# Performance work log

Measured on AMD Instinct MI355X. Metric: run time of the kernel, lower is better.

The kernel has to match this reference:

```python
import jax, jax.numpy as jnp
import numpy as np

GROUPS = 32
EPS = 1e-5

def setup_inputs() -> dict:
    key = jax.random.key(0)
    k1, k2, k3 = jax.random.split(key, 3)
    C = 512
    x = jax.random.normal(k1, (4, C, 64, 64), dtype=jnp.float32)
    gn_weight = jnp.ones((C,), jnp.float32)
    gn_bias = jnp.zeros((C,), jnp.float32)
    qkv_weight = jax.random.normal(k2, (3 * C, C), jnp.float32) * (1.0 / np.sqrt(C))
    proj_weight = jax.random.normal(k3, (C, C), jnp.float32) * (1.0 / np.sqrt(C))
    proj_bias = jnp.zeros((C,), jnp.float32)
    return {"x": x, "gn_weight": gn_weight, "gn_bias": gn_bias,
            "qkv_weight": qkv_weight, "proj_weight": proj_weight, "proj_bias": proj_bias}

def reference(x, gn_weight, gn_bias, qkv_weight, proj_weight, proj_bias):
    n, c, h, w = x.shape
    residue = x
    # GroupNorm(32, c): normalize over (c//32 channels * h * w) per group
    xg = x.reshape(n, GROUPS, -1)
    mu = xg.mean(axis=-1, keepdims=True)
    var = xg.var(axis=-1, keepdims=True)
    xn = (xg - mu) * jax.lax.rsqrt(var + EPS)
    xn = xn.reshape(n, c, h, w) * gn_weight[None, :, None, None] + gn_bias[None, :, None, None]
    # tokens: [n, T, c] with T = h*w
    t = xn.reshape(n, c, h * w).transpose(0, 2, 1)
    # qkv linear (no bias), n_heads = 1 so head_size = c
    qkv = jnp.einsum('ntc,dc->ntd', t, qkv_weight)
    q, k, v = jnp.split(qkv, 3, axis=-1)
    scale = 1.0 / np.sqrt(c)
    scores = jnp.einsum('nqc,nkc->nqk', q, k) * scale  # [n, T, T]
    weights = jax.nn.softmax(scores, axis=-1)
    out = jnp.einsum('nqk,nkc->nqc', weights, v)
    out = jnp.einsum('ntc,dc->ntd', out, proj_weight) + proj_bias
    out = out.transpose(0, 2, 1).reshape(n, c, h, w)
    return out + residue
```

## Files before the change

kernel.cpp:

```cpp
#include <hip/hip_runtime.h>
#include <hip/hip_bf16.h>

typedef __bf16 bf16;
typedef __bf16 bf16x8 __attribute__((ext_vector_type(8)));
typedef float f32x4 __attribute__((ext_vector_type(4)));

__device__ __forceinline__ void gload_lds16(const bf16* g, bf16* l) {
    __builtin_amdgcn_global_load_lds(
        (const __attribute__((address_space(1))) void*)g,
        (__attribute__((address_space(3))) void*)l, 16, 0, 0);
}

__global__ __launch_bounds__(256) void k_gnstats(const float* __restrict__ x,
                                                 float2* __restrict__ stats) {
    const int g = blockIdx.x;
    const float4* p = (const float4*)(x + (long)g * 65536);
    float s = 0.f, ss = 0.f;
    #pragma unroll 8
    for (int i = 0; i < 64; ++i) {
        float4 v = p[threadIdx.x + i * 256];
        s  += v.x + v.y + v.z + v.w;
        ss += v.x * v.x + v.y * v.y + v.z * v.z + v.w * v.w;
    }
    #pragma unroll
    for (int off = 32; off >= 1; off >>= 1) {
        s  += __shfl_down(s, off);
        ss += __shfl_down(ss, off);
    }
    __shared__ float rs[4], rss[4];
    if ((threadIdx.x & 63) == 0) { rs[threadIdx.x >> 6] = s; rss[threadIdx.x >> 6] = ss; }
    __syncthreads();
    if (threadIdx.x == 0) {
        float S  = rs[0] + rs[1] + rs[2] + rs[3];
        float SS = rss[0] + rss[1] + rss[2] + rss[3];
        float mu = S * (1.f / 65536.f);
        float var = SS * (1.f / 65536.f) - mu * mu;
        stats[g] = make_float2(mu, rsqrtf(var + 1e-5f));
    }
}

__global__ __launch_bounds__(256) void k_norm_t(const float* __restrict__ x,
                                                const float* __restrict__ w,
                                                const float* __restrict__ b,
                                                const float2* __restrict__ stats,
                                                bf16* __restrict__ t) {
    __shared__ float tile[64][65];
    const int bid = blockIdx.x;
    const int n = bid >> 9, rem = bid & 511;
    const int s0 = (rem >> 3) * 64, c0 = (rem & 7) * 64;
    const int tid = threadIdx.x;
    const int sl = tid & 63, cq = tid >> 6;
    #pragma unroll
    for (int i = 0; i < 16; ++i) {
        const int cl = cq * 16 + i;
        const int c = c0 + cl;
        const float2 st = stats[n * 32 + (c >> 4)];
        const float v = x[((long)(n * 512 + c)) * 4096 + s0 + sl];
        tile[cl][sl] = (v - st.x) * st.y * w[c] + b[c];
    }
    __syncthreads();
    #pragma unroll
    for (int i = 0; i < 16; ++i) {
        const int sl2 = cq * 16 + i;
        const int cl2 = tid & 63;
        t[((long)(n * 4096 + s0 + sl2)) * 512 + c0 + cl2] = (bf16)tile[cl2][sl2];
    }
}

__global__ __launch_bounds__(256) void k_convw(const float* __restrict__ qw,
                                               const float* __restrict__ pw,
                                               bf16* __restrict__ qwb,
                                               bf16* __restrict__ pwb) {
    const int i = blockIdx.x * 256 + threadIdx.x;
    if (i < 786432) {
        float v = qw[i];
        if (i < 512 * 512) v *= 0.06376281516217733f;
        qwb[i] = (bf16)v;
    } else {
        const int j = i - 786432;
        pwb[j] = (bf16)pw[j];
    }
}

__global__ __launch_bounds__(256) void k_vt(const bf16* __restrict__ qkv,
                                            bf16* __restrict__ Vt) {
    __shared__ bf16 tile[64][66];
    const int bid = blockIdx.x;
    const int n = bid >> 9, rem = bid & 511;
    const int s0 = (rem >> 3) * 64, d0 = (rem & 7) * 64;
    const int tid = threadIdx.x;
    #pragma unroll
    for (int i = 0; i < 16; ++i) {
        const int sl = (tid >> 6) * 16 + i;
        const int dl = tid & 63;
        tile[sl][dl] = qkv[((long)(n * 4096 + s0 + sl)) * 1536 + 1024 + d0 + dl];
    }
    __syncthreads();
    #pragma unroll
    for (int i = 0; i < 16; ++i) {
        const int dl = (tid >> 6) * 16 + i;
        const int sl = tid & 63;
        Vt[((long)(n * 512 + d0 + dl)) * 4096 + s0 + sl] = tile[sl][dl];
    }
}

__global__ __launch_bounds__(512, 1) void k_flashpv(
    const bf16* __restrict__ S, const bf16* __restrict__ Vt,
    bf16* __restrict__ O) {
    __shared__ bf16 Bs[2][512 * 64];
    __shared__ bf16 As[64 * 64];
    __shared__ float sstat[64];
    const int t = threadIdx.x;
    const int w = t >> 6, l = t & 63, lr = l & 15, lg = l >> 4;
    const int r = t >> 3, c8 = t & 7, r7 = r & 7;
    const int lr7 = lr & 7;
    const long z = blockIdx.y;
    const int bx = blockIdx.x;

    const bf16* Sg = S + z * ((long)4096 * 4096) + (long)(bx * 64 + r) * 4096 + c8 * 8;
    const bf16* Vg = Vt + z * ((long)512 * 4096) + (long)r * 4096 + (c8 ^ r7) * 8;

    auto issueB = [&](int tile, int buf) {
        bf16* lp = Bs[buf];
        #pragma unroll
        for (int u = 0; u < 8; ++u)
            gload_lds16(Vg + (long)u * 64 * 4096 + tile * 64, lp + u * 4096 + t * 8);
    };

    f32x4 acc[4][4];
    #pragma unroll
    for (int i = 0; i < 4; ++i)
        #pragma unroll
        for (int n = 0; n < 4; ++n) acc[i][n] = f32x4{0.f, 0.f, 0.f, 0.f};

    float m_run = -1e30f, l_run = 0.f;
    bf16x8 pa;
    float scale = 0.f;

    auto stats = [&](bf16x8 sv) {
        float fv[8];
        #pragma unroll
        for (int j = 0; j < 8; ++j) fv[j] = (float)sv[j];
        float tmax = fv[0];
        #pragma unroll
        for (int j = 1; j < 8; ++j) tmax = fmaxf(tmax, fv[j]);
        tmax = fmaxf(tmax, __shfl_xor(tmax, 1));
        tmax = fmaxf(tmax, __shfl_xor(tmax, 2));
        tmax = fmaxf(tmax, __shfl_xor(tmax, 4));
        float mnew, scl;
        if (tmax > m_run + 8.f) { mnew = tmax; scl = exp2f(m_run - tmax); }
        else                    { mnew = m_run; scl = 1.f; }
        float ts = 0.f;
        #pragma unroll
        for (int j = 0; j < 8; ++j) { fv[j] = exp2f(fv[j] - mnew); ts += fv[j]; }
        ts += __shfl_xor(ts, 1);
        ts += __shfl_xor(ts, 2);
        ts += __shfl_xor(ts, 4);
        l_run = l_run * scl + ts;
        m_run = mnew;
        #pragma unroll
        for (int j = 0; j < 8; ++j) pa[j] = (bf16)fv[j];
        scale = scl;
    };

    bf16x8 sv0 = *(const bf16x8*)(Sg);
    issueB(0, 0);
    stats(sv0);

    for (int ti = 0; ti < 64; ++ti) {
        __builtin_amdgcn_s_barrier();
        asm volatile("" ::: "memory");
        *(bf16x8*)(As + r * 64 + ((c8 ^ r7) * 8)) = pa;
        if (c8 == 0) sstat[r] = scale;
        bf16x8 sv;
        if (ti < 63) {
            sv = *(const bf16x8*)(Sg + (ti + 1) * 64);
            issueB(ti + 1, (ti + 1) & 1);
            asm volatile("s_waitcnt vmcnt(9) lgkmcnt(0)" ::: "memory");
        } else {
            asm volatile("s_waitcnt vmcnt(0) lgkmcnt(0)" ::: "memory");
        }
        __builtin_amdgcn_sched_barrier(0);
        __builtin_amdgcn_s_barrier();
        asm volatile("" ::: "memory");

        #pragma unroll
        for (int mi = 0; mi < 4; ++mi) {
            float4 sc = *(const float4*)&sstat[mi * 16 + lg * 4];
            if (sc.x != 1.f || sc.y != 1.f || sc.z != 1.f || sc.w != 1.f) {
                f32x4 scv = {sc.x, sc.y, sc.z, sc.w};
                #pragma unroll
                for (int n = 0; n < 4; ++n) acc[mi][n] *= scv;
            }
        }

        const bf16* Bsb = Bs[ti & 1];
        __builtin_amdgcn_s_setprio(1);
        #pragma unroll
        for (int kk = 0; kk < 2; ++kk) {
            bf16x8 af[4], bf[4];
            #pragma unroll
            for (int mi = 0; mi < 4; ++mi)
                af[mi] = *(const bf16x8*)(As + (mi * 16 + lr) * 64 + (((kk * 4 + lg) ^ lr7) * 8));
            #pragma unroll
            for (int n = 0; n < 4; ++n)
                bf[n] = *(const bf16x8*)(Bsb + (w * 64 + n * 16 + lr) * 64 + (((kk * 4 + lg) ^ lr7) * 8));
            #pragma unroll
            for (int mi = 0; mi < 4; ++mi)
                #pragma unroll
                for (int n = 0; n < 4; ++n)
                    acc[mi][n] = __builtin_amdgcn_mfma_f32_16x16x32_bf16(af[mi], bf[n], acc[mi][n], 0, 0, 0);
        }
        __builtin_amdgcn_s_setprio(0);

        if (ti < 63) stats(sv);
    }

    __builtin_amdgcn_s_barrier();
    asm volatile("" ::: "memory");
    if (c8 == 0) sstat[r] = l_run;
    asm volatile("s_waitcnt lgkmcnt(0)" ::: "memory");
    __builtin_amdgcn_s_barrier();
    asm volatile("" ::: "memory");

    bf16* Oz = O + z * ((long)4096 * 512);
    #pragma unroll
    for (int mi = 0; mi < 4; ++mi) {
        float4 lv = *(const float4*)&sstat[mi * 16 + lg * 4];
        float inv0 = 1.f / lv.x, inv1 = 1.f / lv.y, inv2 = 1.f / lv.z, inv3 = 1.f / lv.w;
        #pragma unroll
        for (int n = 0; n < 4; ++n) {
            const long base = (long)(bx * 64 + mi * 16 + lg * 4) * 512 + w * 64 + n * 16 + lr;
            Oz[base]           = (bf16)(acc[mi][n][0] * inv0);
            Oz[base + 512]     = (bf16)(acc[mi][n][1] * inv1);
            Oz[base + 1024]    = (bf16)(acc[mi][n][2] * inv2);
            Oz[base + 1536]    = (bf16)(acc[mi][n][3] * inv3);
        }
    }
}

#define PH(mh, kk, S_, WN)                                                         \
  {                                                                                \
    if ((mh) == 0) {                                                               \
      _Pragma("unroll")                                                            \
      for (int n = 0; n < 4; ++n) {                                                \
        int row = wn * 64 + n * 16 + lr;                                           \
        int cg = lg ^ (row & 3);                                                   \
        bfr[n] = *(const bf16x8*)(BsT + (kk) * 8192 + row * 32 + cg * 8);          \
      }                                                                            \
    }                                                                              \
    _Pragma("unroll")                                                              \
    for (int i = 0; i < 4; ++i) {                                                  \
      int row = wm * 128 + ((mh) * 4 + i) * 16 + lr;                               \
      int cg = lg ^ (row & 3);                                                     \
      af[i] = *(const bf16x8*)(AsT + (kk) * 8192 + row * 32 + cg * 8);             \
    }                                                                              \
    if ((S_) >= 0) issue_unit(S_);                                                 \
    __builtin_amdgcn_s_barrier();                                                  \
    asm volatile("" ::: "memory");                                                 \
    __builtin_amdgcn_s_setprio(1);                                                 \
    _Pragma("unroll")                                                              \
    for (int i = 0; i < 4; ++i)                                                    \
      _Pragma("unroll")                                                            \
      for (int n = 0; n < 4; ++n)                                                  \
        acc[(mh) * 4 + i][n] =                                                     \
            __builtin_amdgcn_mfma_f32_16x16x32_bf16(af[i], bfr[n],                 \
                                                    acc[(mh) * 4 + i][n], 0, 0, 0);\
    __builtin_amdgcn_s_setprio(0);                                                 \
    if constexpr ((WN) >= 0)                                                       \
      asm volatile("s_waitcnt vmcnt(%0)" ::"i"(WN) : "memory");                    \
    __builtin_amdgcn_s_barrier();                                                  \
    asm volatile("" ::: "memory");                                                 \
  }

__global__ __launch_bounds__(512, 2) void gemm256(
    const bf16* __restrict__ A, int lda, long aZ,
    const bf16* __restrict__ B, int ldb, long bZ,
    bf16* __restrict__ C, int ldc, long cZ, int K) {
    __shared__ bf16 As[2 * 2 * 256 * 32];
    __shared__ bf16 Bs[2 * 2 * 256 * 32];
    const int t = threadIdx.x;
    const int wid = t >> 6, l = t & 63;
    const int wm = wid >> 2, wn = wid & 3;
    const int lr = l & 15;
    const int lg = l >> 4;
    const long z = blockIdx.z;

    const int gx = gridDim.x;
    int nwg = gx * gridDim.y;
    int flat = blockIdx.y * gx + blockIdx.x;
    if ((nwg & 7) == 0) { int qq = nwg >> 3; flat = (flat & 7) * qq + (flat >> 3); }
    const int bx = flat % gx, by = flat / gx;

    const bf16* Ab = A + z * aZ + (long)bx * 256 * lda;
    const bf16* Bb = B + z * bZ + (long)by * 256 * ldb;

    const int NT = K >> 6;
    const int NT4 = NT << 2;

    f32x4 acc[8][4];
    #pragma unroll
    for (int i = 0; i < 8; ++i)
        #pragma unroll
        for (int n = 0; n < 4; ++n) acc[i][n] = f32x4{0.f, 0.f, 0.f, 0.f};

    const int srow = t >> 2;
    const int scg0 = t & 3;

    auto issue_unit = [&](int s) {
        int ti = s >> 2, idx = s & 3;
        int kh = idx >> 1, isB = idx & 1;
        const bf16* g = isB ? Bb : Ab;
        int ld = isB ? ldb : lda;
        bf16* lp = (isB ? Bs : As) + ((ti & 1) * 2 + kh) * 8192;
        int k0 = ti * 64 + kh * 32;
        #pragma unroll
        for (int j = 0; j < 2; ++j) {
            int row = j * 128 + srow;
            int cg = scg0 ^ (row & 3);
            gload_lds16(g + (long)row * ld + k0 + cg * 8, lp + (j * 512 + t) * 8);
        }
    };

    #pragma unroll
    for (int s = 0; s < 6; ++s) issue_unit(s);
    asm volatile("s_waitcnt vmcnt(8)" ::: "memory");
    __builtin_amdgcn_s_barrier();
    asm volatile("" ::: "memory");

    bf16x8 bfr[4], af[4];

    for (int ti = 0; ti < NT - 2; ++ti) {
        const bf16* AsT = As + (ti & 1) * 16384;
        const bf16* BsT = Bs + (ti & 1) * 16384;
        const int sb = 4 * ti + 6;
        PH(0, 0, sb + 0, -1)
        PH(1, 0, sb + 1, 8)
        PH(0, 1, sb + 2, -1)
        PH(1, 1, sb + 3, 8)
    }
    {
        const bf16* AsT = As + ((NT - 2) & 1) * 16384;
        const bf16* BsT = Bs + ((NT - 2) & 1) * 16384;
        PH(0, 0, NT4 - 2, -1)
        PH(1, 0, NT4 - 1, 8)
        PH(0, 1, -1, -1)
        PH(1, 1, -1, 4)
    }
    {
        const bf16* AsT = As + ((NT - 1) & 1) * 16384;
        const bf16* BsT = Bs + ((NT - 1) & 1) * 16384;
        PH(0, 0, -1, -1)
        PH(1, 0, -1, 0)
        PH(0, 1, -1, -1)
        PH(1, 1, -1, -1)
    }

    const int row0 = bx * 256 + wm * 128;
    const int col0 = by * 256 + wn * 64;
    const int rq = lg * 4;
    bf16* Cz = C + z * cZ;
    #pragma unroll
    for (int i = 0; i < 8; ++i)
        #pragma unroll
        for (int n = 0; n < 4; ++n) {
            const int col = col0 + n * 16 + lr;
            #pragma unroll
            for (int r = 0; r < 4; ++r)
                Cz[(long)(row0 + i * 16 + rq + r) * ldc + col] = (bf16)acc[i][n][r];
        }
}

#define PH128(nh, kk, S_, WN)                                                      \
  {                                                                                \
    if ((nh) == 0) {                                                               \
      _Pragma("unroll")                                                            \
      for (int i = 0; i < 4; ++i) {                                                \
        int row = wm * 64 + i * 16 + lr;                                           \
        int cg = lg ^ (row & 3);                                                   \
        af[i] = *(const bf16x8*)(AsT + (kk) * 8192 + row * 32 + cg * 8);           \
      }                                                                            \
    }                                                                              \
    _Pragma("unroll")                                                              \
    for (int j = 0; j < 2; ++j) {                                                  \
      int row = wn * 64 + ((nh) * 2 + j) * 16 + lr;                                \
      int cg = lg ^ (row & 3);                                                     \
      bfr[j] = *(const bf16x8*)(BsT + (kk) * 4096 + row * 32 + cg * 8);            \
    }                                                                              \
    if ((S_) >= 0) issue_unit(S_);                                                 \
    __builtin_amdgcn_s_barrier();                                                  \
    asm volatile("" ::: "memory");                                                 \
    __builtin_amdgcn_s_setprio(1);                                                 \
    _Pragma("unroll")                                                              \
    for (int i = 0; i < 4; ++i)                                                    \
      _Pragma("unroll")                                                            \
      for (int j = 0; j < 2; ++j)                                                  \
        acc[i][(nh) * 2 + j] =                                                     \
            __builtin_amdgcn_mfma_f32_16x16x32_bf16(af[i], bfr[j],                 \
                                                    acc[i][(nh) * 2 + j], 0, 0, 0);\
    __builtin_amdgcn_s_setprio(0);                                                 \
    if constexpr ((WN) >= 0)                                                       \
      asm volatile("s_waitcnt vmcnt(%0)" ::"i"(WN) : "memory");                    \
    __builtin_amdgcn_s_barrier();                                                  \
    asm volatile("" ::: "memory");                                                 \
  }

template <int EPI>
__global__ __launch_bounds__(512, 2) void gemm_n128(
    const bf16* __restrict__ A, int lda, long aZ,
    const bf16* __restrict__ B, int ldb, long bZ,
    void* __restrict__ Cvp, int ldc, long cZ, int K,
    const float* __restrict__ bias) {
    __shared__ bf16 As[2 * 2 * 256 * 32];
    __shared__ bf16 Bs[2 * 2 * 128 * 32];
    const int t = threadIdx.x;
    const int wid = t >> 6, l = t & 63;
    const int wm = wid >> 1, wn = wid & 1;
    const int lr = l & 15;
    const int lg = l >> 4;
    const long z = blockIdx.z;

    const int gx = gridDim.x;
    int nwg = gx * gridDim.y;
    int flat = blockIdx.y * gx + blockIdx.x;
    if ((nwg & 7) == 0) { int qq = nwg >> 3; flat = (flat & 7) * qq + (flat >> 3); }
    const int bx = flat % gx, by = flat / gx;

    const bf16* Ab = A + z * aZ + (long)bx * 256 * lda;
    const bf16* Bb = B + z * bZ + (long)by * 128 * ldb;

    const int NT = K >> 6;
    const int NT4 = NT << 2;

    f32x4 acc[4][4];
    #pragma unroll
    for (int i = 0; i < 4; ++i)
        #pragma unroll
        for (int n = 0; n < 4; ++n) acc[i][n] = f32x4{0.f, 0.f, 0.f, 0.f};

    const int srow = t >> 2;
    const int scg0 = t & 3;

    auto issue_unit = [&](int s) {
        int ti = s >> 2, idx = s & 3;
        int kh = idx >> 1, isB = idx & 1;
        int k0 = ti * 64 + kh * 32;
        if (isB) {
            bf16* lp = Bs + ((ti & 1) * 2 + kh) * 4096;
            int cg = scg0 ^ (srow & 3);
            gload_lds16(Bb + (long)srow * ldb + k0 + cg * 8, lp + t * 8);
        } else {
            bf16* lp = As + ((ti & 1) * 2 + kh) * 8192;
            #pragma unroll
            for (int j = 0; j < 2; ++j) {
                int row = j * 128 + srow;
                int cg = scg0 ^ (row & 3);
                gload_lds16(Ab + (long)row * lda + k0 + cg * 8, lp + (j * 512 + t) * 8);
            }
        }
    };

    #pragma unroll
    for (int s = 0; s < 6; ++s) issue_unit(s);
    asm volatile("s_waitcnt vmcnt(6)" ::: "memory");
    __builtin_amdgcn_s_barrier();
    asm volatile("" ::: "memory");

    bf16x8 bfr[2], af[4];

    for (int ti = 0; ti < NT - 2; ++ti) {
        const bf16* AsT = As + (ti & 1) * 16384;
        const bf16* BsT = Bs + (ti & 1) * 8192;
        const int sb = 4 * ti + 6;
        PH128(0, 0, sb + 0, -1)
        PH128(1, 0, sb + 1, 6)
        PH128(0, 1, sb + 2, -1)
        PH128(1, 1, sb + 3, 6)
    }
    {
        const bf16* AsT = As + ((NT - 2) & 1) * 16384;
        const bf16* BsT = Bs + ((NT - 2) & 1) * 8192;
        PH128(0, 0, NT4 - 2, -1)
        PH128(1, 0, NT4 - 1, 6)
        PH128(0, 1, -1, -1)
        PH128(1, 1, -1, 3)
    }
    {
        const bf16* AsT = As + ((NT - 1) & 1) * 16384;
        const bf16* BsT = Bs + ((NT - 1) & 1) * 8192;
        PH128(0, 0, -1, -1)
        PH128(1, 0, -1, 0)
        PH128(0, 1, -1, -1)
        PH128(1, 1, -1, -1)
    }

    const int row0 = bx * 256 + wm * 64;
    const int col0 = by * 128 + wn * 64;
    const int rq = lg * 4;
    if (EPI == 2) {
        float* C = (float*)Cvp + z * cZ;
        #pragma unroll
        for (int i = 0; i < 4; ++i)
            #pragma unroll
            for (int n = 0; n < 4; ++n) {
                const int col = col0 + n * 16 + lr;
                #pragma unroll
                for (int r = 0; r < 4; ++r)
                    C[(long)(row0 + i * 16 + rq + r) * ldc + col] = acc[i][n][r] + bias[col];
            }
    } else {
        bf16* C = (bf16*)Cvp + z * cZ;
        #pragma unroll
        for (int i = 0; i < 4; ++i)
            #pragma unroll
            for (int n = 0; n < 4; ++n) {
                const int col = col0 + n * 16 + lr;
                #pragma unroll
                for (int r = 0; r < 4; ++r)
                    C[(long)(row0 + i * 16 + rq + r) * ldc + col] = (bf16)acc[i][n][r];
            }
    }
}

__global__ __launch_bounds__(256) void k_final(const float* __restrict__ pb,
                                               const float* __restrict__ x,
                                               float* __restrict__ out) {
    __shared__ float tile[64][65];
    const int bid = blockIdx.x;
    const int n = bid >> 9, rem = bid & 511;
    const int s0 = (rem >> 3) * 64, c0 = (rem & 7) * 64;
    const int tid = threadIdx.x;
    #pragma unroll
    for (int i = 0; i < 16; ++i) {
        const int sl = (tid >> 6) * 16 + i;
        const int cl = tid & 63;
        tile[sl][cl] = pb[((long)(n * 4096 + s0 + sl)) * 512 + c0 + cl];
    }
    __syncthreads();
    #pragma unroll
    for (int i = 0; i < 16; ++i) {
        const int cl = (tid >> 6) * 16 + i;
        const int sl = tid & 63;
        const long oi = ((long)(n * 512 + c0 + cl)) * 4096 + s0 + sl;
        out[oi] = tile[sl][cl] + x[oi];
    }
}

extern "C" void kernel_launch(void* const* d_in, const int* in_sizes, int n_in,
                              void* d_out, int out_size, void* d_ws, size_t ws_size,
                              hipStream_t stream) {
    const float* x     = (const float*)d_in[0];
    const float* gnw   = (const float*)d_in[1];
    const float* gnb   = (const float*)d_in[2];
    const float* qkvw  = (const float*)d_in[3];
    const float* projw = (const float*)d_in[4];
    const float* projb = (const float*)d_in[5];

    char* ws = (char*)d_ws;
    size_t off = 0;
    auto alloc = [&](size_t bytes) {
        void* p = ws + off;
        off += (bytes + 255) & ~(size_t)255;
        return p;
    };
    bf16*   qwb   = (bf16*)alloc((size_t)1536 * 512 * 2);
    bf16*   pwb   = (bf16*)alloc((size_t)512 * 512 * 2);
    float2* stats = (float2*)alloc((size_t)128 * 8);
    bf16*   tbuf  = (bf16*)alloc((size_t)16384 * 512 * 2);
    bf16*   qkv   = (bf16*)alloc((size_t)16384 * 1536 * 2);
    bf16*   Vt    = (bf16*)alloc((size_t)4 * 512 * 4096 * 2);
    const size_t SSZ = (size_t)4096 * 4096 * 2;
    const size_t fixed = off;
    int g = 1;
    if (ws_size >= fixed + 4 * SSZ) g = 4;
    else if (ws_size >= fixed + 2 * SSZ) g = 2;
    bf16* Sbuf = (bf16*)alloc(g * SSZ);

    k_gnstats<<<128, 256, 0, stream>>>(x, stats);
    k_norm_t<<<2048, 256, 0, stream>>>(x, gnw, gnb, stats, tbuf);
    k_convw<<<4096, 256, 0, stream>>>(qkvw, projw, qwb, pwb);

    gemm256<<<dim3(64, 6, 1), 512, 0, stream>>>(
        tbuf, 512, 0, qwb, 512, 0, qkv, 1536, 0, 512);

    k_vt<<<2048, 256, 0, stream>>>(qkv, Vt);

    const long TS = (long)4096 * 1536;
    for (int g0 = 0; g0 < 4; g0 += g) {
        gemm256<<<dim3(16, 16, g), 512, 0, stream>>>(
            qkv + (long)g0 * TS, 1536, TS,
            qkv + (long)g0 * TS + 512, 1536, TS,
            Sbuf, 4096, (long)4096 * 4096, 512);
        k_flashpv<<<dim3(64, g), 512, 0, stream>>>(
            Sbuf, Vt + (long)g0 * 512 * 4096, tbuf + (long)g0 * 4096 * 512);
    }

    gemm_n128<2><<<dim3(64, 4, 1), 512, 0, stream>>>(
        tbuf, 512, 0, pwb, 512, 0, (float*)Sbuf, 512, 0, 512, projb);

    k_final<<<2048, 256, 0, stream>>>((float*)Sbuf, x, (float*)d_out);
}
```

Baseline: 331.4 us.

## Split flash PV kernel across two head-dimension halves with 256-thread blocks

Measured after the change: 337.7 us. About the same (+1.9%).

```diff
diff --git a/kernel.cpp b/kernel.cpp
--- a/kernel.cpp
+++ b/kernel.cpp
@@ -104,27 +104,29 @@
     }
 }
 
-__global__ __launch_bounds__(512, 1) void k_flashpv(
+__global__ __launch_bounds__(256, 2) void k_flashpv(
     const bf16* __restrict__ S, const bf16* __restrict__ Vt,
     bf16* __restrict__ O) {
-    __shared__ bf16 Bs[2][512 * 64];
+    __shared__ bf16 Bs[2][256 * 64];
     __shared__ bf16 As[64 * 64];
     __shared__ float sstat[64];
     const int t = threadIdx.x;
     const int w = t >> 6, l = t & 63, lr = l & 15, lg = l >> 4;
-    const int r = t >> 3, c8 = t & 7, r7 = r & 7;
+    const int r = t >> 2, c4 = t & 3, r7 = r & 7;
+    const int vr = t >> 3, vc8 = t & 7, vr7 = vr & 7;
     const int lr7 = lr & 7;
-    const long z = blockIdx.y;
+    const long z = blockIdx.z;
     const int bx = blockIdx.x;
-
-    const bf16* Sg = S + z * ((long)4096 * 4096) + (long)(bx * 64 + r) * 4096 + c8 * 8;
-    const bf16* Vg = Vt + z * ((long)512 * 4096) + (long)r * 4096 + (c8 ^ r7) * 8;
+    const int dh = blockIdx.y;
+
+    const bf16* Sg = S + z * ((long)4096 * 4096) + (long)(bx * 64 + r) * 4096 + c4 * 16;
+    const bf16* Vg = Vt + z * ((long)512 * 4096) + (long)(dh * 256 + vr) * 4096 + (vc8 ^ vr7) * 8;
 
     auto issueB = [&](int tile, int buf) {
         bf16* lp = Bs[buf];
         #pragma unroll
         for (int u = 0; u < 8; ++u)
-            gload_lds16(Vg + (long)u * 64 * 4096 + tile * 64, lp + u * 4096 + t * 8);
+            gload_lds16(Vg + (long)u * 32 * 4096 + tile * 64, lp + u * 2048 + t * 8);
     };
 
     f32x4 acc[4][4];
@@ -134,49 +136,50 @@
         for (int n = 0; n < 4; ++n) acc[i][n] = f32x4{0.f, 0.f, 0.f, 0.f};
 
     float m_run = -1e30f, l_run = 0.f;
-    bf16x8 pa;
+    bf16x8 pa0, pa1;
     float scale = 0.f;
 
-    auto stats = [&](bf16x8 sv) {
-        float fv[8];
-        #pragma unroll
-        for (int j = 0; j < 8; ++j) fv[j] = (float)sv[j];
+    auto stats = [&](bf16x8 sa, bf16x8 sb) {
+        float fv[16];
+        #pragma unroll
+        for (int j = 0; j < 8; ++j) { fv[j] = (float)sa[j]; fv[8 + j] = (float)sb[j]; }
         float tmax = fv[0];
         #pragma unroll
-        for (int j = 1; j < 8; ++j) tmax = fmaxf(tmax, fv[j]);
+        for (int j = 1; j < 16; ++j) tmax = fmaxf(tmax, fv[j]);
         tmax = fmaxf(tmax, __shfl_xor(tmax, 1));
         tmax = fmaxf(tmax, __shfl_xor(tmax, 2));
-        tmax = fmaxf(tmax, __shfl_xor(tmax, 4));
         float mnew, scl;
         if (tmax > m_run + 8.f) { mnew = tmax; scl = exp2f(m_run - tmax); }
         else                    { mnew = m_run; scl = 1.f; }
         float ts = 0.f;
         #pragma unroll
-        for (int j = 0; j < 8; ++j) { fv[j] = exp2f(fv[j] - mnew); ts += fv[j]; }
+        for (int j = 0; j < 16; ++j) { fv[j] = exp2f(fv[j] - mnew); ts += fv[j]; }
         ts += __shfl_xor(ts, 1);
         ts += __shfl_xor(ts, 2);
-        ts += __shfl_xor(ts, 4);
         l_run = l_run * scl + ts;
         m_run = mnew;
         #pragma unroll
-        for (int j = 0; j < 8; ++j) pa[j] = (bf16)fv[j];
+        for (int j = 0; j < 8; ++j) { pa0[j] = (bf16)fv[j]; pa1[j] = (bf16)fv[8 + j]; }
         scale = scl;
     };
 
-    bf16x8 sv0 = *(const bf16x8*)(Sg);
+    bf16x8 sa0 = *(const bf16x8*)(Sg);
+    bf16x8 sb0 = *(const bf16x8*)(Sg + 8);
     issueB(0, 0);
-    stats(sv0);
+    stats(sa0, sb0);
 
     for (int ti = 0; ti < 64; ++ti) {
         __builtin_amdgcn_s_barrier();
         asm volatile("" ::: "memory");
-        *(bf16x8*)(As + r * 64 + ((c8 ^ r7) * 8)) = pa;
-        if (c8 == 0) sstat[r] = scale;
-        bf16x8 sv;
+        *(bf16x8*)(As + r * 64 + (((c4 * 2) ^ r7) * 8)) = pa0;
+        *(bf16x8*)(As + r * 64 + (((c4 * 2 + 1) ^ r7) * 8)) = pa1;
+        if (c4 == 0) sstat[r] = scale;
+        bf16x8 sa, sb;
         if (ti < 63) {
-            sv = *(const bf16x8*)(Sg + (ti + 1) * 64);
+            sa = *(const bf16x8*)(Sg + (ti + 1) * 64);
+            sb = *(const bf16x8*)(Sg + (ti + 1) * 64 + 8);
             issueB(ti + 1, (ti + 1) & 1);
-            asm volatile("s_waitcnt vmcnt(9) lgkmcnt(0)" ::: "memory");
+            asm volatile("s_waitcnt vmcnt(10) lgkmcnt(0)" ::: "memory");
         } else {
             asm volatile("s_waitcnt vmcnt(0) lgkmcnt(0)" ::: "memory");
         }
@@ -213,12 +216,12 @@
         }
         __builtin_amdgcn_s_setprio(0);
 
-        if (ti < 63) stats(sv);
+        if (ti < 63) stats(sa, sb);
     }
 
     __builtin_amdgcn_s_barrier();
     asm volatile("" ::: "memory");
-    if (c8 == 0) sstat[r] = l_run;
+    if (c4 == 0) sstat[r] = l_run;
     asm volatile("s_waitcnt lgkmcnt(0)" ::: "memory");
     __builtin_amdgcn_s_barrier();
     asm volatile("" ::: "memory");
@@ -230,7 +233,7 @@
         float inv0 = 1.f / lv.x, inv1 = 1.f / lv.y, inv2 = 1.f / lv.z, inv3 = 1.f / lv.w;
         #pragma unroll
         for (int n = 0; n < 4; ++n) {
-            const long base = (long)(bx * 64 + mi * 16 + lg * 4) * 512 + w * 64 + n * 16 + lr;
+            const long base = (long)(bx * 64 + mi * 16 + lg * 4) * 512 + dh * 256 + w * 64 + n * 16 + lr;
             Oz[base]           = (bf16)(acc[mi][n][0] * inv0);
             Oz[base + 512]     = (bf16)(acc[mi][n][1] * inv1);
             Oz[base + 1024]    = (bf16)(acc[mi][n][2] * inv2);
@@ -591,7 +594,7 @@
             qkv + (long)g0 * TS, 1536, TS,
             qkv + (long)g0 * TS + 512, 1536, TS,
             Sbuf, 4096, (long)4096 * 4096, 512);
-        k_flashpv<<<dim3(64, g), 512, 0, stream>>>(
+        k_flashpv<<<dim3(64, 2, g), 256, 0, stream>>>(
             Sbuf, Vt + (long)g0 * 512 * 4096, tbuf + (long)g0 * 4096 * 512);
     }
 
```

## Fuse exp and row-sum into QK^T GEMM epilogue, make PV a plain GEMM

Applied to the files above, without the earlier changes.

After: 312.5 us. 5.7% less time.

```diff
diff --git a/kernel.cpp b/kernel.cpp
--- a/kernel.cpp
+++ b/kernel.cpp
@@ -101,141 +101,6 @@
         const int dl = (tid >> 6) * 16 + i;
         const int sl = tid & 63;
         Vt[((long)(n * 512 + d0 + dl)) * 4096 + s0 + sl] = tile[sl][dl];
-    }
-}
-
-__global__ __launch_bounds__(512, 1) void k_flashpv(
-    const bf16* __restrict__ S, const bf16* __restrict__ Vt,
-    bf16* __restrict__ O) {
-    __shared__ bf16 Bs[2][512 * 64];
-    __shared__ bf16 As[64 * 64];
-    __shared__ float sstat[64];
-    const int t = threadIdx.x;
-    const int w = t >> 6, l = t & 63, lr = l & 15, lg = l >> 4;
-    const int r = t >> 3, c8 = t & 7, r7 = r & 7;
-    const int lr7 = lr & 7;
-    const long z = blockIdx.y;
-    const int bx = blockIdx.x;
-
-    const bf16* Sg = S + z * ((long)4096 * 4096) + (long)(bx * 64 + r) * 4096 + c8 * 8;
-    const bf16* Vg = Vt + z * ((long)512 * 4096) + (long)r * 4096 + (c8 ^ r7) * 8;
-
-    auto issueB = [&](int tile, int buf) {
-        bf16* lp = Bs[buf];
-        #pragma unroll
-        for (int u = 0; u < 8; ++u)
-            gload_lds16(Vg + (long)u * 64 * 4096 + tile * 64, lp + u * 4096 + t * 8);
-    };
-
-    f32x4 acc[4][4];
-    #pragma unroll
-    for (int i = 0; i < 4; ++i)
-        #pragma unroll
-        for (int n = 0; n < 4; ++n) acc[i][n] = f32x4{0.f, 0.f, 0.f, 0.f};
-
-    float m_run = -1e30f, l_run = 0.f;
-    bf16x8 pa;
-    float scale = 0.f;
-
-    auto stats = [&](bf16x8 sv) {
-        float fv[8];
-        #pragma unroll
-        for (int j = 0; j < 8; ++j) fv[j] = (float)sv[j];
-        float tmax = fv[0];
-        #pragma unroll
-        for (int j = 1; j < 8; ++j) tmax = fmaxf(tmax, fv[j]);
-        tmax = fmaxf(tmax, __shfl_xor(tmax, 1));
-        tmax = fmaxf(tmax, __shfl_xor(tmax, 2));
-        tmax = fmaxf(tmax, __shfl_xor(tmax, 4));
-        float mnew, scl;
-        if (tmax > m_run + 8.f) { mnew = tmax; scl = exp2f(m_run - tmax); }
-        else                    { mnew = m_run; scl = 1.f; }
-        float ts = 0.f;
-        #pragma unroll
-        for (int j = 0; j < 8; ++j) { fv[j] = exp2f(fv[j] - mnew); ts += fv[j]; }
-        ts += __shfl_xor(ts, 1);
-        ts += __shfl_xor(ts, 2);
-        ts += __shfl_xor(ts, 4);
-        l_run = l_run * scl + ts;
-        m_run = mnew;
-        #pragma unroll
-        for (int j = 0; j < 8; ++j) pa[j] = (bf16)fv[j];
-        scale = scl;
-    };
-
-    bf16x8 sv0 = *(const bf16x8*)(Sg);
-    issueB(0, 0);
-    stats(sv0);
-
-    for (int ti = 0; ti < 64; ++ti) {
-        __builtin_amdgcn_s_barrier();
-        asm volatile("" ::: "memory");
-        *(bf16x8*)(As + r * 64 + ((c8 ^ r7) * 8)) = pa;
-        if (c8 == 0) sstat[r] = scale;
-        bf16x8 sv;
-        if (ti < 63) {
-            sv = *(const bf16x8*)(Sg + (ti + 1) * 64);
-            issueB(ti + 1, (ti + 1) & 1);
-            asm volatile("s_waitcnt vmcnt(9) lgkmcnt(0)" ::: "memory");
-        } else {
-            asm volatile("s_waitcnt vmcnt(0) lgkmcnt(0)" ::: "memory");
-        }
-        __builtin_amdgcn_sched_barrier(0);
-        __builtin_amdgcn_s_barrier();
-        asm volatile("" ::: "memory");
-
-        #pragma unroll
-        for (int mi = 0; mi < 4; ++mi) {
-            float4 sc = *(const float4*)&sstat[mi * 16 + lg * 4];
-            if (sc.x != 1.f || sc.y != 1.f || sc.z != 1.f || sc.w != 1.f) {
-                f32x4 scv = {sc.x, sc.y, sc.z, sc.w};
-                #pragma unroll
-                for (int n = 0; n < 4; ++n) acc[mi][n] *= scv;
-            }
-        }
-
-        const bf16* Bsb = Bs[ti & 1];
-        __builtin_amdgcn_s_setprio(1);
-        #pragma unroll
-        for (int kk = 0; kk < 2; ++kk) {
-            bf16x8 af[4], bf[4];
-            #pragma unroll
-            for (int mi = 0; mi < 4; ++mi)
-                af[mi] = *(const bf16x8*)(As + (mi * 16 + lr) * 64 + (((kk * 4 + lg) ^ lr7) * 8));
-            #pragma unroll
-            for (int n = 0; n < 4; ++n)
-                bf[n] = *(const bf16x8*)(Bsb + (w * 64 + n * 16 + lr) * 64 + (((kk * 4 + lg) ^ lr7) * 8));
-            #pragma unroll
-            for (int mi = 0; mi < 4; ++mi)
-                #pragma unroll
-                for (int n = 0; n < 4; ++n)
-                    acc[mi][n] = __builtin_amdgcn_mfma_f32_16x16x32_bf16(af[mi], bf[n], acc[mi][n], 0, 0, 0);
-        }
-        __builtin_amdgcn_s_setprio(0);
-
-        if (ti < 63) stats(sv);
-    }
-
-    __builtin_amdgcn_s_barrier();
-    asm volatile("" ::: "memory");
-    if (c8 == 0) sstat[r] = l_run;
-    asm volatile("s_waitcnt lgkmcnt(0)" ::: "memory");
-    __builtin_amdgcn_s_barrier();
-    asm volatile("" ::: "memory");
-
-    bf16* Oz = O + z * ((long)4096 * 512);
-    #pragma unroll
-    for (int mi = 0; mi < 4; ++mi) {
-        float4 lv = *(const float4*)&sstat[mi * 16 + lg * 4];
-        float inv0 = 1.f / lv.x, inv1 = 1.f / lv.y, inv2 = 1.f / lv.z, inv3 = 1.f / lv.w;
-        #pragma unroll
-        for (int n = 0; n < 4; ++n) {
-            const long base = (long)(bx * 64 + mi * 16 + lg * 4) * 512 + w * 64 + n * 16 + lr;
-            Oz[base]           = (bf16)(acc[mi][n][0] * inv0);
-            Oz[base + 512]     = (bf16)(acc[mi][n][1] * inv1);
-            Oz[base + 1024]    = (bf16)(acc[mi][n][2] * inv2);
-            Oz[base + 1536]    = (bf16)(acc[mi][n][3] * inv3);
-        }
     }
 }
 
@@ -273,10 +138,12 @@
     asm volatile("" ::: "memory");                                                 \
   }
 
+template <int EPI>
 __global__ __launch_bounds__(512, 2) void gemm256(
     const bf16* __restrict__ A, int lda, long aZ,
     const bf16* __restrict__ B, int ldb, long bZ,
-    bf16* __restrict__ C, int ldc, long cZ, int K) {
+    bf16* __restrict__ C, int ldc, long cZ, int K,
+    float* __restrict__ Lp) {
     __shared__ bf16 As[2 * 2 * 256 * 32];
     __shared__ bf16 Bs[2 * 2 * 256 * 32];
     const int t = threadIdx.x;
@@ -360,15 +227,146 @@
     const int col0 = by * 256 + wn * 64;
     const int rq = lg * 4;
     bf16* Cz = C + z * cZ;
-    #pragma unroll
-    for (int i = 0; i < 8; ++i)
+
+    if (EPI == 1) {
+        float rs[8][4];
+        #pragma unroll
+        for (int i = 0; i < 8; ++i)
+            #pragma unroll
+            for (int r = 0; r < 4; ++r) rs[i][r] = 0.f;
+        #pragma unroll
+        for (int i = 0; i < 8; ++i)
+            #pragma unroll
+            for (int n = 0; n < 4; ++n) {
+                const int col = col0 + n * 16 + lr;
+                #pragma unroll
+                for (int r = 0; r < 4; ++r) {
+                    float p = exp2f(acc[i][n][r]);
+                    rs[i][r] += p;
+                    Cz[(long)(row0 + i * 16 + rq + r) * ldc + col] = (bf16)p;
+                }
+            }
+        #pragma unroll
+        for (int i = 0; i < 8; ++i)
+            #pragma unroll
+            for (int r = 0; r < 4; ++r) {
+                float s = rs[i][r];
+                s += __shfl_xor(s, 1);
+                s += __shfl_xor(s, 2);
+                s += __shfl_xor(s, 4);
+                s += __shfl_xor(s, 8);
+                rs[i][r] = s;
+            }
+        float* lsf = (float*)As;
+        if (lr == 0) {
+            #pragma unroll
+            for (int i = 0; i < 8; ++i)
+                #pragma unroll
+                for (int r = 0; r < 4; ++r)
+                    lsf[wn * 256 + wm * 128 + i * 16 + lg * 4 + r] = rs[i][r];
+        }
+        __syncthreads();
+        if (t < 256) {
+            float v = lsf[t] + lsf[256 + t] + lsf[512 + t] + lsf[768 + t];
+            Lp[((long)z * 16 + by) * 4096 + bx * 256 + t] = v;
+        }
+    } else {
+        #pragma unroll
+        for (int i = 0; i < 8; ++i)
+            #pragma unroll
+            for (int n = 0; n < 4; ++n) {
+                const int col = col0 + n * 16 + lr;
+                #pragma unroll
+                for (int r = 0; r < 4; ++r)
+                    Cz[(long)(row0 + i * 16 + rq + r) * ldc + col] = (bf16)acc[i][n][r];
+            }
+    }
+}
+
+__global__ __launch_bounds__(512, 1) void k_pv(
+    const bf16* __restrict__ P, const float* __restrict__ Lp,
+    const bf16* __restrict__ Vt, bf16* __restrict__ O) {
+    __shared__ bf16 Bs[2][512 * 64];
+    __shared__ bf16 As[2][64 * 64];
+    __shared__ float linv[64];
+    const int t = threadIdx.x;
+    const int w = t >> 6, l = t & 63, lr = l & 15, lg = l >> 4;
+    const int lr7 = lr & 7;
+    const int sr = t >> 3, sc8 = t & 7, sr7 = sr & 7;
+    const long z = blockIdx.y;
+    const int bx = blockIdx.x;
+
+    const bf16* Pg = P + z * ((long)4096 * 4096) + (long)(bx * 64 + sr) * 4096 + (sc8 ^ sr7) * 8;
+    const bf16* Vg = Vt + z * ((long)512 * 4096) + (long)sr * 4096 + (sc8 ^ sr7) * 8;
+
+    auto issue = [&](int tile, int buf) {
+        gload_lds16(Pg + tile * 64, As[buf] + t * 8);
+        #pragma unroll
+        for (int u = 0; u < 8; ++u)
+            gload_lds16(Vg + (long)u * 64 * 4096 + tile * 64, Bs[buf] + u * 4096 + t * 8);
+    };
+
+    if (t < 64) {
+        const float* lpp = Lp + z * 16 * 4096 + bx * 64 + t;
+        float s = 0.f;
+        #pragma unroll
+        for (int j = 0; j < 16; ++j) s += lpp[j * 4096];
+        linv[t] = 1.f / s;
+    }
+
+    f32x4 acc[4][4];
+    #pragma unroll
+    for (int i = 0; i < 4; ++i)
+        #pragma unroll
+        for (int n = 0; n < 4; ++n) acc[i][n] = f32x4{0.f, 0.f, 0.f, 0.f};
+
+    issue(0, 0);
+    issue(1, 1);
+
+    for (int ti = 0; ti < 64; ++ti) {
+        if (ti < 63) { asm volatile("s_waitcnt vmcnt(9)" ::: "memory"); }
+        else         { asm volatile("s_waitcnt vmcnt(0)" ::: "memory"); }
+        __builtin_amdgcn_s_barrier();
+        asm volatile("" ::: "memory");
+
+        const bf16* Asb = As[ti & 1];
+        const bf16* Bsb = Bs[ti & 1];
+        __builtin_amdgcn_s_setprio(1);
+        #pragma unroll
+        for (int kk = 0; kk < 2; ++kk) {
+            bf16x8 af[4], bfv[4];
+            #pragma unroll
+            for (int mi = 0; mi < 4; ++mi)
+                af[mi] = *(const bf16x8*)(Asb + (mi * 16 + lr) * 64 + (((kk * 4 + lg) ^ lr7) * 8));
+            #pragma unroll
+            for (int n = 0; n < 4; ++n)
+                bfv[n] = *(const bf16x8*)(Bsb + (w * 64 + n * 16 + lr) * 64 + (((kk * 4 + lg) ^ lr7) * 8));
+            #pragma unroll
+            for (int mi = 0; mi < 4; ++mi)
+                #pragma unroll
+                for (int n = 0; n < 4; ++n)
+                    acc[mi][n] = __builtin_amdgcn_mfma_f32_16x16x32_bf16(af[mi], bfv[n], acc[mi][n], 0, 0, 0);
+        }
+        __builtin_amdgcn_s_setprio(0);
+
+        __builtin_amdgcn_s_barrier();
+        asm volatile("" ::: "memory");
+        if (ti < 62) issue(ti + 2, ti & 1);
+    }
+
+    bf16* Oz = O + z * ((long)4096 * 512);
+    #pragma unroll
+    for (int mi = 0; mi < 4; ++mi) {
+        float4 lv = *(const float4*)&linv[mi * 16 + lg * 4];
         #pragma unroll
         for (int n = 0; n < 4; ++n) {
-            const int col = col0 + n * 16 + lr;
-            #pragma unroll
-            for (int r = 0; r < 4; ++r)
-                Cz[(long)(row0 + i * 16 + rq + r) * ldc + col] = (bf16)acc[i][n][r];
+            const long base = (long)(bx * 64 + mi * 16 + lg * 4) * 512 + w * 64 + n * 16 + lr;
+            Oz[base]        = (bf16)(acc[mi][n][0] * lv.x);
+            Oz[base + 512]  = (bf16)(acc[mi][n][1] * lv.y);
+            Oz[base + 1024] = (bf16)(acc[mi][n][2] * lv.z);
+            Oz[base + 1536] = (bf16)(acc[mi][n][3] * lv.w);
         }
+    }
 }
 
 #define PH128(nh, kk, S_, WN)                                                      \
@@ -569,6 +567,7 @@
     bf16*   tbuf  = (bf16*)alloc((size_t)16384 * 512 * 2);
     bf16*   qkv   = (bf16*)alloc((size_t)16384 * 1536 * 2);
     bf16*   Vt    = (bf16*)alloc((size_t)4 * 512 * 4096 * 2);
+    float*  Lpart = (float*)alloc((size_t)4 * 16 * 4096 * 4);
     const size_t SSZ = (size_t)4096 * 4096 * 2;
     const size_t fixed = off;
     int g = 1;
@@ -580,19 +579,19 @@
     k_norm_t<<<2048, 256, 0, stream>>>(x, gnw, gnb, stats, tbuf);
     k_convw<<<4096, 256, 0, stream>>>(qkvw, projw, qwb, pwb);
 
-    gemm256<<<dim3(64, 6, 1), 512, 0, stream>>>(
-        tbuf, 512, 0, qwb, 512, 0, qkv, 1536, 0, 512);
+    gemm256<0><<<dim3(64, 6, 1), 512, 0, stream>>>(
+        tbuf, 512, 0, qwb, 512, 0, qkv, 1536, 0, 512, nullptr);
 
     k_vt<<<2048, 256, 0, stream>>>(qkv, Vt);
 
     const long TS = (long)4096 * 1536;
     for (int g0 = 0; g0 < 4; g0 += g) {
-        gemm256<<<dim3(16, 16, g), 512, 0, stream>>>(
+        gemm256<1><<<dim3(16, 16, g), 512, 0, stream>>>(
             qkv + (long)g0 * TS, 1536, TS,
             qkv + (long)g0 * TS + 512, 1536, TS,
-            Sbuf, 4096, (long)4096 * 4096, 512);
-        k_flashpv<<<dim3(64, g), 512, 0, stream>>>(
-            Sbuf, Vt + (long)g0 * 512 * 4096, tbuf + (long)g0 * 4096 * 512);
+            Sbuf, 4096, (long)4096 * 4096, 512, Lpart);
+        k_pv<<<dim3(64, g), 512, 0, stream>>>(
+            Sbuf, Lpart, Vt + (long)g0 * 512 * 4096, tbuf + (long)g0 * 4096 * 512);
     }
 
     gemm_n128<2><<<dim3(64, 4, 1), 512, 0, stream>>>(
```
